# Kernel tuning notes

Hardware: AMD Instinct MI355X
Metric: run time of the kernel (lower is better)

## Reference

```python
import jax, jax.numpy as jnp
import numpy as np

N_E = 512
E_DIM = 128
LEGACY = 0.2
B, T = 64, 1024


def setup_inputs() -> dict:
    key = jax.random.key(0)
    k1, k2 = jax.random.split(key, 2)
    key_soft = jax.random.normal(k1, (B, T, E_DIM), dtype=jnp.float32)
    emb_weight = jax.random.uniform(k2, (N_E + 1, E_DIM), dtype=jnp.float32,
                                    minval=-1.0 / N_E, maxval=1.0 / N_E)
    zero_ts_mask = jnp.zeros((B,), dtype=jnp.bool_)
    return {"key_soft": key_soft, "emb_weight": emb_weight, "zero_ts_mask": zero_ts_mask}


def _neighbor_indices(d, zero_ts_mask, n_e):
    # d: [B, T, n_e+1] (no grad needed; only used for int index selection)
    ind0 = jnp.clip(jnp.argmin(d[:, 0, :], axis=1), 0, n_e - 1)
    ind0 = jnp.where(zero_ts_mask, 0, ind0)

    def step(ind, d_t):  # ind: [B], d_t: [B, n_e+1]
        d_here = jnp.take_along_axis(d_t, ind[:, None], axis=1)[:, 0]
        ind_next = jnp.clip(ind + 1, 0, n_e - 1)
        d_next = jnp.take_along_axis(d_t, ind_next[:, None], axis=1)[:, 0]
        ind_new = jnp.where(d_here <= d_next, ind, ind_next)
        return ind_new, ind_new

    _, rest = jax.lax.scan(step, ind0, jnp.swapaxes(d[:, 1:, :], 0, 1))  # [T-1, B]
    return jnp.concatenate([ind0[None, :], rest], axis=0).T  # [B, T]


def reference(key_soft, emb_weight, zero_ts_mask):
    sg = jax.lax.stop_gradient
    n_e = emb_weight.shape[0] - 1
    b, t, e_dim = key_soft.shape

    # squared-distance matrix: [B, T, n_e+1]
    d = (jnp.sum(key_soft ** 2, axis=-1, keepdims=True)
         + jnp.sum(emb_weight ** 2, axis=1)
         - 2.0 * jnp.einsum('btd,nd->btn', key_soft, emb_weight))
    d_ng = sg(d)

    min_indices = jnp.argmin(d_ng, axis=-1)                 # [B, T] (over full n_e+1)
    enc = _neighbor_indices(d_ng, zero_ts_mask, n_e)        # [B, T]

    key_hard_here = emb_weight[enc]                                  # [B, T, D]
    key_hard_next = emb_weight[jnp.clip(enc + 1, 0, n_e - 1)]        # [B, T, D]
    key_min = emb_weight[min_indices]                                # [B, T, D]

    def vq_loss(kh):
        return (jnp.sum((sg(key_soft) - kh) ** 2, axis=-1)
                + jnp.sum((key_soft - sg(kh)) ** 2, axis=-1) * LEGACY)

    loss_here_base = vq_loss(key_hard_here)
    loss_next_base = vq_loss(key_hard_next)

    energy = (jnp.sum((sg(key_soft) - key_hard_next) ** 2, axis=-1)
              - jnp.sum((sg(key_soft) - key_hard_here) ** 2, axis=-1)
              + (jnp.sum((key_soft - sg(key_hard_next)) ** 2, axis=-1)
                 - jnp.sum((key_soft - sg(key_hard_here)) ** 2, axis=-1)) * LEGACY)

    change = (enc[:, 1:] - enc[:, :-1]) != 0
    same_hard_mask = jnp.where(change, 0.0, 1.0)
    energy_change = (energy[:, 1:] - energy[:, :-1]) * same_hard_mask
    loss_energy_descent = jnp.maximum(energy_change + 1e-06 / n_e,
                                      jnp.zeros_like(energy_change)).mean()
    energy_mean = energy.mean()

    loss_min_indices = vq_loss(key_min)
    loss_min_here = jnp.where(loss_min_indices < loss_here_base, loss_min_indices, 0.0)
    loss_min_next = jnp.where(loss_min_indices < loss_next_base, loss_min_indices, 0.0)

    loss_here = loss_here_base - loss_next_base - loss_min_here
    loss_next = loss_next_base - loss_here_base - loss_min_next

    key_hard = key_soft + sg(key_hard_here - key_soft)  # straight-through

    v = jnp.max(jnp.max(enc, axis=1) - jnp.min(enc, axis=1))
    return (key_hard, enc, v, loss_here, loss_next, energy_mean, loss_energy_descent)
```

## Files before the change

### kernel.cpp

```cpp
#include <hip/hip_runtime.h>
#include <cfloat>
#include <cstdint>

#define B_  64
#define T_  1024
#define D_  128
#define NE  512
#define P_  (B_*T_)

#define O_KH   0
#define O_ENC  (P_*D_)
#define O_V    (O_ENC + P_)
#define O_LH   (O_V + 1)
#define O_LN   (O_LH + P_)
#define O_EM   (O_LN + P_)
#define O_LED  (O_EM + 1)

typedef __attribute__((ext_vector_type(8))) short bf16x8;
typedef __attribute__((ext_vector_type(4))) float floatx4;
typedef unsigned long long u64;

__device__ __forceinline__ void pack8(const float4& a, const float4& b,
                                      uint4& h, uint4& l)
{
    float v[8] = {a.x,a.y,a.z,a.w,b.x,b.y,b.z,b.w};
    unsigned hw[4], lw[4];
    #pragma unroll
    for (int e = 0; e < 4; e++) {
        const unsigned ua = __float_as_uint(v[2*e]);
        const unsigned ub = __float_as_uint(v[2*e+1]);
        const float fa = __uint_as_float(ua & 0xffff0000u);
        const float fb = __uint_as_float(ub & 0xffff0000u);
        const unsigned da = __float_as_uint(v[2*e]   - fa);
        const unsigned db = __float_as_uint(v[2*e+1] - fb);
        hw[e] = (ub & 0xffff0000u) | (ua >> 16);
        lw[e] = (db & 0xffff0000u) | (da >> 16);
    }
    h = make_uint4(hw[0],hw[1],hw[2],hw[3]);
    l = make_uint4(lw[0],lw[1],lw[2],lw[3]);
}

__device__ __forceinline__ u64 shflx64(u64 v, int d)
{
    const int lo = __shfl_xor((int)(unsigned)(v & 0xffffffffULL), d);
    const int hi = __shfl_xor((int)(unsigned)(v >> 32), d);
    return ((u64)(unsigned)hi << 32) | (unsigned)lo;
}

__device__ __forceinline__ unsigned sortkey(float f)
{
    const unsigned b = __float_as_uint(f);
    return b ^ (unsigned)(((int)b >> 31) | (int)0x80000000);
}

__global__ __launch_bounds__(256) void kFG(const float* __restrict__ emb,
                                           unsigned short* __restrict__ ehi,
                                           unsigned short* __restrict__ elo,
                                           float* __restrict__ sq)
{
    const int t = blockIdx.x * 256 + threadIdx.x;
    const int n = t >> 2, kst = t & 3;
    const float4* src = (const float4*)(emb + (size_t)n * D_ + kst * 32);
    float ss = 0.f;
    #pragma unroll
    for (int g = 0; g < 4; g++) {
        const float4 a = src[2*g], b = src[2*g+1];
        ss += a.x*a.x + a.y*a.y + a.z*a.z + a.w*a.w
            + b.x*b.x + b.y*b.y + b.z*b.z + b.w*b.w;
        uint4 h, l;
        pack8(a, b, h, l);
        const int f = ((n >> 4) * 4 + kst) * 4 + g;
        *(uint4*)(ehi + (size_t)f*128 + (size_t)(n & 15)*8) = h;
        *(uint4*)(elo + (size_t)f*128 + (size_t)(n & 15)*8) = l;
    }
    ss += __shfl_xor(ss, 1);
    ss += __shfl_xor(ss, 2);
    if (kst == 0) sq[n] = ss;
}

__global__ __launch_bounds__(256) void kA(const float* __restrict__ ks,
                                          const float* __restrict__ sq,
                                          const unsigned short* __restrict__ ehi,
                                          const unsigned short* __restrict__ elo,
                                          u64* __restrict__ bits,
                                          float* __restrict__ sfirst,
                                          float* __restrict__ slast,
                                          unsigned* __restrict__ mins,
                                          unsigned short* __restrict__ mini16)
{
    const int tid  = threadIdx.x;
    const int lane = tid & 63;
    const int wv   = tid >> 6;
    const int m    = lane & 15;
    const int q    = lane >> 4;
    const int pt   = blockIdx.x & 1023;
    const int p0   = pt * 64;
    const int ch   = (blockIdx.x >> 10) * 4 + wv;
    const int nb   = ch * 64;

    floatx4 acc[4][4];
    #pragma unroll
    for (int i = 0; i < 4; i++)
        #pragma unroll
        for (int j = 0; j < 4; j++)
            #pragma unroll
            for (int r = 0; r < 4; r++) acc[i][j][r] = 0.f;

    bf16x8 ah[4], al[4], bh[4], bl[4];
    float4 F[8];

    auto loadA = [&](int kst) {
        #pragma unroll
        for (int i = 0; i < 4; i++) {
            const int off = (((ch*4 + i) * 4 + kst) * 4 + q) * 128 + m*8;
            ah[i] = *(const bf16x8*)(ehi + off);
            al[i] = *(const bf16x8*)(elo + off);
        }
    };
    auto issueB = [&](int kst) {
        #pragma unroll
        for (int j = 0; j < 4; j++) {
            const float4* src = (const float4*)(ks + (size_t)(p0 + j*16 + m)*D_
                                                + kst*32 + q*8);
            F[2*j]   = src[0];
            F[2*j+1] = src[1];
        }
    };
    auto packB = [&]() {
        #pragma unroll
        for (int j = 0; j < 4; j++) {
            uint4 h, l;
            pack8(F[2*j], F[2*j+1], h, l);
            bh[j] = *(const bf16x8*)&h;
            bl[j] = *(const bf16x8*)&l;
        }
    };
    auto mfma3 = [&]() {
        #pragma unroll
        for (int i = 0; i < 4; i++)
            #pragma unroll
            for (int j = 0; j < 4; j++)
                acc[i][j] = __builtin_amdgcn_mfma_f32_16x16x32_bf16(ah[i], bh[j], acc[i][j], 0, 0, 0);
        #pragma unroll
        for (int i = 0; i < 4; i++)
            #pragma unroll
            for (int j = 0; j < 4; j++)
                acc[i][j] = __builtin_amdgcn_mfma_f32_16x16x32_bf16(ah[i], bl[j], acc[i][j], 0, 0, 0);
        #pragma unroll
        for (int i = 0; i < 4; i++)
            #pragma unroll
            for (int j = 0; j < 4; j++)
                acc[i][j] = __builtin_amdgcn_mfma_f32_16x16x32_bf16(al[i], bh[j], acc[i][j], 0, 0, 0);
    };

    issueB(0);
    loadA(0);
    packB();
    issueB(1);
    mfma3();
    loadA(1);
    packB();
    issueB(2);
    mfma3();
    loadA(2);
    packB();
    issueB(3);
    mfma3();
    loadA(3);
    packB();
    mfma3();

    float sa[4][4];
    #pragma unroll
    for (int i = 0; i < 4; i++) {
        const float4 s4 = *(const float4*)(sq + nb + i*16 + q*4);
        sa[i][0]=s4.x; sa[i][1]=s4.y; sa[i][2]=s4.z; sa[i][3]=s4.w;
    }
    #pragma unroll
    for (int j = 0; j < 4; j++) {
        float S[4][4];
        #pragma unroll
        for (int i = 0; i < 4; i++)
            #pragma unroll
            for (int r = 0; r < 4; r++)
                S[i][r] = fmaf(-2.f, acc[i][j][r], sa[i][r]);

        float nq[4], ni[4];
        #pragma unroll
        for (int i = 0; i < 4; i++) nq[i] = __shfl_down(S[i][0], 16);
        #pragma unroll
        for (int i = 0; i < 3; i++) ni[i] = __shfl(S[i+1][0], m);
        ni[3] = 0.f;

        u64 w = 0;
        #pragma unroll
        for (int i = 0; i < 4; i++) {
            #pragma unroll
            for (int r = 0; r < 3; r++)
                w |= (u64)(S[i][r] <= S[i][r+1]) << (16*i + 4*q + r);
            if (!(i == 3 && q == 3)) {
                const float nxt = (q < 3) ? nq[i] : ni[i];
                w |= (u64)(S[i][3] <= nxt) << (16*i + 4*q + 3);
            }
        }
        if (ch == 7 && q == 3) w |= 1ULL << 63;
        w |= shflx64(w, 16);
        w |= shflx64(w, 32);

        float mv = S[0][0]; int mi_ = nb + q*4;
        #pragma unroll
        for (int i = 0; i < 4; i++)
            #pragma unroll
            for (int r = 0; r < 4; r++) {
                if (i == 0 && r == 0) continue;
                const int nid = nb + 16*i + 4*q + r;
                if (S[i][r] < mv) { mv = S[i][r]; mi_ = nid; }
            }
        #pragma unroll
        for (int d = 16; d <= 32; d <<= 1) {
            const float v2 = __shfl_xor(mv, d);
            const int   i2 = __shfl_xor(mi_, d);
            if (v2 < mv || (v2 == mv && i2 < mi_)) { mv = v2; mi_ = i2; }
        }

        const size_t pg = (size_t)(p0 + j*16 + m);
        if (q == 0) {
            bits  [pg*8 + ch] = w;
            sfirst[pg*8 + ch] = S[0][0];
            mins  [pg*8 + ch] = sortkey(mv);
            mini16[pg*8 + ch] = (unsigned short)mi_;
        }
        if (q == 3) slast[pg*8 + ch] = S[3][3];
    }
}

struct KBwin { u64 W[8]; float F[8]; float L[8]; };

__global__ __launch_bounds__(64) void kB(const float* __restrict__ ks,
                                         const float* __restrict__ emb,
                                         const unsigned char* __restrict__ mask,
                                         const u64* __restrict__ bits,
                                         const float* __restrict__ sfirst,
                                         const float* __restrict__ slast,
                                         const unsigned* __restrict__ mins,
                                         const unsigned short* __restrict__ mini16,
                                         int* __restrict__ enci,
                                         float* __restrict__ out)
{
    const int b    = blockIdx.x;
    const int lane = threadIdx.x;
    const size_t p0 = (size_t)b * T_;

    const float2 e = ((const float2*)(emb + (size_t)512*D_))[lane];
    const float2 k = ((const float2*)(ks  + p0*D_))[lane];
    float s5 = e.x*(e.x - 2.f*k.x) + e.y*(e.y - 2.f*k.y);
    #pragma unroll
    for (int m = 32; m >= 1; m >>= 1) s5 += __shfl_xor(s5, m);

    u64 kk = ~0ULL;
    if (lane < 8)       kk = ((u64)mins[p0*8 + lane] << 32) | (u64)mini16[p0*8 + lane];
    else if (lane == 8) kk = ((u64)sortkey(s5) << 32) | 512ULL;
    #pragma unroll
    for (int d = 1; d <= 8; d <<= 1) {
        const u64 o = shflx64(kk, d);
        kk = (o < kk) ? o : kk;
    }
    const int mi = __shfl((int)(unsigned)(kk & 0xffffffffULL), 0);
    int cur = (mi < NE) ? mi : NE - 1;
    if (mask[b]) cur = 0;
    if (lane == 0) { enci[p0] = cur; out[O_ENC + p0] = (float)cur; }

    KBwin wa, wb;

    auto loadwin = [&](KBwin& d, int t0) {
        const int t = t0 + lane;
        if (t < T_) {
            const ulonglong2* bp = (const ulonglong2*)(bits + (p0 + t)*8);
            const ulonglong2 w01 = bp[0], w23 = bp[1], w45 = bp[2], w67 = bp[3];
            d.W[0]=w01.x; d.W[1]=w01.y; d.W[2]=w23.x; d.W[3]=w23.y;
            d.W[4]=w45.x; d.W[5]=w45.y; d.W[6]=w67.x; d.W[7]=w67.y;
            const float4* fp = (const float4*)(sfirst + (p0 + t)*8);
            const float4 f0 = fp[0], f1 = fp[1];
            d.F[0]=f0.x; d.F[1]=f0.y; d.F[2]=f0.z; d.F[3]=f0.w;
            d.F[4]=f1.x; d.F[5]=f1.y; d.F[6]=f1.z; d.F[7]=f1.w;
            const float4* lp = (const float4*)(slast + (p0 + t)*8);
            const float4 l0 = lp[0], l1 = lp[1];
            d.L[0]=l0.x; d.L[1]=l0.y; d.L[2]=l0.z; d.L[3]=l0.w;
            d.L[4]=l1.x; d.L[5]=l1.y; d.L[6]=l1.z; d.L[7]=l1.w;
        } else {
            #pragma unroll
            for (int c = 0; c < 8; c++) { d.W[c] = ~0ULL; d.F[c] = 1.f; d.L[c] = 0.f; }
        }
    };

    auto scanwin = [&](KBwin& d, int t0) {
        #pragma unroll
        for (int c = 0; c < 7; c++)
            d.W[c] |= (u64)(d.L[c] <= d.F[c+1]) << 63;

        const int w0   = cur >> 6;
        const int off0 = cur & 63;
        u64 a = d.W[0];
        #pragma unroll
        for (int c = 1; c < 8; c++) a = (w0 == c) ? d.W[c] : a;
        u64 bn = ~0ULL;
        #pragma unroll
        for (int c = 1; c < 8; c++) bn = (w0 == c-1) ? d.W[c] : bn;
        const u64 u = (off0 == 0) ? a : ((a >> off0) | (bn << (64 - off0)));

        const unsigned ulo = (unsigned)u;
        const unsigned uhi = (unsigned)(u >> 32);
        int doff = 0;
        int myenc = cur;
        #pragma unroll
        for (int j = 0; j < 64; j++) {
            const unsigned slo = (unsigned)__builtin_amdgcn_readlane((int)ulo, j);
            const unsigned shi = (unsigned)__builtin_amdgcn_readlane((int)uhi, j);
            const u64 word = ((u64)shi << 32) | slo;
            const int bit = (int)((word >> doff) & 1ULL);
            doff += 1 - bit;
            if (lane == j) myenc = cur + doff;
        }
        cur += doff;
        const int t = t0 + lane;
        if (t < T_) {
            enci[p0 + t] = myenc;
            out[O_ENC + p0 + t] = (float)myenc;
        }
    };

    loadwin(wa, 1);
    #pragma unroll 1
    for (int wp = 0; wp < 8; wp++) {
        const int t0a = 1 + wp*128;
        loadwin(wb, t0a + 64);
        scanwin(wa, t0a);
        if (wp < 7) loadwin(wa, t0a + 128);
        scanwin(wb, t0a + 64);
    }
}

__global__ __launch_bounds__(256) void kC(const float* __restrict__ ks,
                                          const float* __restrict__ emb,
                                          const int* __restrict__ enci,
                                          const unsigned* __restrict__ mins,
                                          const unsigned short* __restrict__ mini16,
                                          float* __restrict__ out,
                                          float* __restrict__ energy)
{
    const int lane = threadIdx.x & 63;
    const size_t p = (size_t)blockIdx.x * 4 + (threadIdx.x >> 6);
    const int q  = lane >> 4;
    const int qm = lane & 15;

    const int eh = enci[p];
    const int en = (eh + 1 < NE) ? eh + 1 : NE - 1;
    const int row = (q == 0) ? eh : ((q == 1) ? en : 512);

    const float4* ksp = (const float4*)(ks + p*D_);
    const float4 k1 = ksp[qm*2], k2 = ksp[qm*2 + 1];
    const float4* ep = (const float4*)(emb + (size_t)row*D_);
    const float4 e1 = ep[qm*2], e2 = ep[qm*2 + 1];

    float d;
    if (q == 3) {
        d = k1.x*k1.x + k1.y*k1.y + k1.z*k1.z + k1.w*k1.w
          + k2.x*k2.x + k2.y*k2.y + k2.z*k2.z + k2.w*k2.w;
    } else {
        d = e1.x*(e1.x - 2.f*k1.x) + e1.y*(e1.y - 2.f*k1.y)
          + e1.z*(e1.z - 2.f*k1.z) + e1.w*(e1.w - 2.f*k1.w)
          + e2.x*(e2.x - 2.f*k2.x) + e2.y*(e2.y - 2.f*k2.y)
          + e2.z*(e2.z - 2.f*k2.z) + e2.w*(e2.w - 2.f*k2.w);
    }
    #pragma unroll
    for (int s = 1; s <= 8; s <<= 1) d += __shfl_xor(d, s);

    const float ph  = __shfl(d, 0);
    const float pn  = __shfl(d, 16);
    const float p5  = __shfl(d, 32);
    const float sqk = __shfl(d, 48);

    u64 kk = ~0ULL;
    if (lane < 8)       kk = ((u64)mins[p*8 + lane] << 32) | (u64)mini16[p*8 + lane];
    else if (lane == 8) kk = ((u64)sortkey(p5) << 32) | 512ULL;
    #pragma unroll
    for (int s = 1; s <= 8; s <<= 1) {
        const u64 o = shflx64(kk, s);
        kk = (o < kk) ? o : kk;
    }
    const int mi = __shfl((int)(unsigned)(kk & 0xffffffffULL), 0);

    float pm;
    if (mi == eh)      pm = ph;
    else if (mi == en) pm = pn;
    else if (mi == 512) pm = p5;
    else {
        const float4* mp = (const float4*)(emb + (size_t)mi*D_);
        const float4 m1 = mp[qm*2], m2 = mp[qm*2 + 1];
        float dm = m1.x*(m1.x - 2.f*k1.x) + m1.y*(m1.y - 2.f*k1.y)
                 + m1.z*(m1.z - 2.f*k1.z) + m1.w*(m1.w - 2.f*k1.w)
                 + m2.x*(m2.x - 2.f*k2.x) + m2.y*(m2.y - 2.f*k2.y)
                 + m2.z*(m2.z - 2.f*k2.z) + m2.w*(m2.w - 2.f*k2.w);
        #pragma unroll
        for (int s = 1; s <= 8; s <<= 1) dm += __shfl_xor(dm, s);
        pm = __shfl(dm, 0);
    }

    if (q == 0) {
        float4 o1, o2;
        o1.x = k1.x + (e1.x - k1.x); o1.y = k1.y + (e1.y - k1.y);
        o1.z = k1.z + (e1.z - k1.z); o1.w = k1.w + (e1.w - k1.w);
        o2.x = k2.x + (e2.x - k2.x); o2.y = k2.y + (e2.y - k2.y);
        o2.z = k2.z + (e2.z - k2.z); o2.w = k2.w + (e2.w - k2.w);
        ((float4*)(out + p*D_))[qm*2]     = o1;
        ((float4*)(out + p*D_))[qm*2 + 1] = o2;
    }

    if (lane == 0) {
        const float lh = 1.2f * (sqk + ph);
        const float ln = 1.2f * (sqk + pn);
        const float lm = 1.2f * (sqk + pm);
        out[O_LH + p] = lh - ln - ((pm < ph) ? lm : 0.f);
        out[O_LN + p] = ln - lh - ((pm < pn) ? lm : 0.f);
        energy[p] = 1.2f * (pn - ph);
    }
}

__global__ __launch_bounds__(256) void kD1(const float* __restrict__ energy,
                                           const int* __restrict__ enci,
                                           double2* __restrict__ part)
{
    __shared__ double sA[256], sB[256];
    const int p = blockIdx.x * 256 + threadIdx.x;
    const float e = energy[p];
    double se = (double)e;
    double sl = 0.0;
    if ((p & (T_-1)) < T_-1) {
        const float ec = (enci[p+1] == enci[p]) ? (energy[p+1] - e) : 0.f;
        sl = (double)fmaxf(ec + (float)(1e-6/512.0), 0.f);
    }
    sA[threadIdx.x] = se; sB[threadIdx.x] = sl;
    __syncthreads();
    for (int s = 128; s >= 1; s >>= 1) {
        if (threadIdx.x < (unsigned)s) {
            sA[threadIdx.x] += sA[threadIdx.x+s];
            sB[threadIdx.x] += sB[threadIdx.x+s];
        }
        __syncthreads();
    }
    if (threadIdx.x == 0) { part[blockIdx.x] = make_double2(sA[0], sB[0]); }
}

__global__ __launch_bounds__(256) void kD2(const double2* __restrict__ part,
                                           const int* __restrict__ enci,
                                           float* __restrict__ out)
{
    __shared__ double sA[256], sB[256];
    const double2 pv = part[threadIdx.x];
    sA[threadIdx.x] = pv.x; sB[threadIdx.x] = pv.y;
    __syncthreads();
    for (int s = 128; s >= 1; s >>= 1) {
        if (threadIdx.x < (unsigned)s) {
            sA[threadIdx.x] += sA[threadIdx.x+s];
            sB[threadIdx.x] += sB[threadIdx.x+s];
        }
        __syncthreads();
    }
    if (threadIdx.x < 64) {
        int v = enci[(size_t)threadIdx.x*T_ + T_-1] - enci[(size_t)threadIdx.x*T_];
        #pragma unroll
        for (int m = 32; m >= 1; m >>= 1) {
            const int v2 = __shfl_xor(v, m);
            v = (v2 > v) ? v2 : v;
        }
        if (threadIdx.x == 0) {
            out[O_V]   = (float)v;
            out[O_EM]  = (float)(sA[0] / (double)P_);
            out[O_LED] = (float)(sB[0] / (double)(B_*(T_-1)));
        }
    }
}

extern "C" void kernel_launch(void* const* d_in, const int* in_sizes, int n_in,
                              void* d_out, int out_size, void* d_ws, size_t ws_size,
                              hipStream_t stream)
{
    const float* ks  = (const float*)d_in[0];
    const float* emb = (const float*)d_in[1];
    const unsigned char* mask = (const unsigned char*)d_in[2];

    float* out = (float*)d_out;
    char* w = (char*)d_ws;
    u64*      bits   = (u64*)     (w);
    float*    sfirst = (float*)   (w + (size_t) 4*1024*1024);
    float*    slast  = (float*)   (w + (size_t) 6*1024*1024);
    unsigned* mins   = (unsigned*)(w + (size_t) 8*1024*1024);
    unsigned short* mini16 = (unsigned short*)(w + (size_t)10*1024*1024);
    int*      enci   = (int*)     (w + (size_t)11*1024*1024);
    float*    energy = (float*)   (w + (size_t)11*1024*1024 + 256*1024);
    float*    sq     = (float*)   (w + (size_t)11*1024*1024 + 512*1024);
    double2*  part   = (double2*) (w + (size_t)11*1024*1024 + 516*1024);
    unsigned short* ehi = (unsigned short*)(w + (size_t)11*1024*1024 + 640*1024);
    unsigned short* elo = (unsigned short*)(w + (size_t)11*1024*1024 + 768*1024);

    kFG<<<8,    256, 0, stream>>>(emb, ehi, elo, sq);
    kA <<<2048, 256, 0, stream>>>(ks, sq, ehi, elo, bits, sfirst, slast, mins, mini16);
    kB <<<B_,   64,  0, stream>>>(ks, emb, mask, bits, sfirst, slast, mins, mini16, enci, out);
    kC <<<P_/4, 256, 0, stream>>>(ks, emb, enci, mins, mini16, out, energy);
    kD1<<<256,  256, 0, stream>>>(energy, enci, part);
    kD2<<<1,    256, 0, stream>>>(part, enci, out);
}
```

Measured before the change: 197.8 us.

## Stage packed bf16 key tile in LDS shared across waves

Each block now loads its 64x128 key_soft tile once, splits it into bf16 hi/lo parts, and stores them in shared memory with an XOR swizzle. All four waves then read their B fragments from LDS instead of each wave reloading the fp32 data from global memory and repacking it. This removes four-fold redundant global loads and conversions. The cost is a block-wide barrier, 32KB of LDS that may limit occupancy, and the loss of the earlier software-pipelined global prefetch.

```diff
diff --git a/kernel.cpp b/kernel.cpp
--- a/kernel.cpp
+++ b/kernel.cpp
@@ -88,6 +88,9 @@
                                           unsigned* __restrict__ mins,
                                           unsigned short* __restrict__ mini16)
 {
+    __shared__ unsigned short Bh[64*128];
+    __shared__ unsigned short Bl[64*128];
+
     const int tid  = threadIdx.x;
     const int lane = tid & 63;
     const int wv   = tid >> 6;
@@ -98,6 +101,21 @@
     const int ch   = (blockIdx.x >> 10) * 4 + wv;
     const int nb   = ch * 64;
 
+    {
+        const int srow = tid >> 2;
+        const int scg  = tid & 3;
+        const float4* sp = (const float4*)(ks + ((size_t)p0 + srow)*D_ + scg*32);
+        #pragma unroll
+        for (int g = 0; g < 4; g++) {
+            uint4 h, l;
+            pack8(sp[2*g], sp[2*g+1], h, l);
+            const int cb = (srow*256 + scg*64 + g*16) ^ ((srow & 7) << 4);
+            *(uint4*)((char*)Bh + cb) = h;
+            *(uint4*)((char*)Bl + cb) = l;
+        }
+    }
+    __syncthreads();
+
     floatx4 acc[4][4];
     #pragma unroll
     for (int i = 0; i < 4; i++)
@@ -107,7 +125,6 @@
             for (int r = 0; r < 4; r++) acc[i][j][r] = 0.f;
 
     bf16x8 ah[4], al[4], bh[4], bl[4];
-    float4 F[8];
 
     auto loadA = [&](int kst) {
         #pragma unroll
@@ -117,22 +134,13 @@
             al[i] = *(const bf16x8*)(elo + off);
         }
     };
-    auto issueB = [&](int kst) {
+    auto loadB = [&](int kst) {
         #pragma unroll
         for (int j = 0; j < 4; j++) {
-            const float4* src = (const float4*)(ks + (size_t)(p0 + j*16 + m)*D_
-                                                + kst*32 + q*8);
-            F[2*j]   = src[0];
-            F[2*j+1] = src[1];
-        }
-    };
-    auto packB = [&]() {
-        #pragma unroll
-        for (int j = 0; j < 4; j++) {
-            uint4 h, l;
-            pack8(F[2*j], F[2*j+1], h, l);
-            bh[j] = *(const bf16x8*)&h;
-            bl[j] = *(const bf16x8*)&l;
+            const int row = j*16 + m;
+            const int cb = (row*256 + kst*64 + q*16) ^ ((row & 7) << 4);
+            bh[j] = *(const bf16x8*)((const char*)Bh + cb);
+            bl[j] = *(const bf16x8*)((const char*)Bl + cb);
         }
     };
     auto mfma3 = [&]() {
@@ -153,22 +161,12 @@
                 acc[i][j] = __builtin_amdgcn_mfma_f32_16x16x32_bf16(al[i], bh[j], acc[i][j], 0, 0, 0);
     };
 
-    issueB(0);
-    loadA(0);
-    packB();
-    issueB(1);
-    mfma3();
-    loadA(1);
-    packB();
-    issueB(2);
-    mfma3();
-    loadA(2);
-    packB();
-    issueB(3);
-    mfma3();
-    loadA(3);
-    packB();
-    mfma3();
+    #pragma unroll
+    for (int kst = 0; kst < 4; kst++) {
+        loadA(kst);
+        loadB(kst);
+        mfma3();
+    }
 
     float sa[4][4];
     #pragma unroll
```

Result: faster. 187.7 us (-5.1%).
